# Optimization experiments

Measured on AMD Instinct MI355X. Metric: run time of the kernel, lower is better.

## Reference

```python
import jax, jax.numpy as jnp
import numpy as np
import math

B, S, D, H = 4, 2048, 1024, 16
DK = D // H


def setup_inputs() -> dict:
    key = jax.random.key(0)
    ks = jax.random.split(key, 5)
    stdv_in = math.sqrt(3.0 / (2 * D))
    stdv_out = math.sqrt(1.0 / D)
    return {
        "query": jax.random.normal(ks[0], (B, S, D), dtype=jnp.float32),
        "key": jax.random.normal(ks[1], (B, S, D), dtype=jnp.float32),
        "value": jax.random.normal(ks[2], (B, S, D), dtype=jnp.float32),
        "input_weight": jax.random.uniform(ks[3], (3, D, D), dtype=jnp.float32, minval=-stdv_in, maxval=stdv_in),
        "output_weight": jax.random.uniform(ks[4], (D, D), dtype=jnp.float32, minval=-stdv_out, maxval=stdv_out),
    }


def reference(query, key, value, input_weight, output_weight):
    # x @ W.T, split into heads: (B,S,D) -> (B,H,S,dk)
    def proj(x, w):
        return (x @ w.T).reshape(B, S, H, DK).transpose(0, 2, 1, 3)

    q = proj(query, input_weight[0])
    k = proj(key, input_weight[1])
    v = proj(value, input_weight[2])

    scores = jnp.einsum("bhqd,bhkd->bhqk", q, k) / math.sqrt(DK)  # (B,H,S,S)
    similarity = jax.nn.softmax(scores, axis=-1)
    attn = jnp.einsum("bhqk,bhkd->bhqd", similarity, v)  # (B,H,S,dk)
    attn = attn.transpose(0, 2, 1, 3).reshape(B, S, D)
    attn = attn @ output_weight.T
    # mean_simi_across_heads=True default
    sim_mean = jnp.mean(similarity, axis=1)  # (B,S,S)
    return attn, sim_mean
```

## Files before the change

kernel.cpp:

```cpp
#include <hip/hip_runtime.h>

typedef _Float16 f16x8 __attribute__((ext_vector_type(8)));
typedef _Float16 f16x4 __attribute__((ext_vector_type(4)));
typedef _Float16 f16x2 __attribute__((ext_vector_type(2)));
typedef __fp16 h16x2 __attribute__((ext_vector_type(2)));
typedef float f32x4 __attribute__((ext_vector_type(4)));

#define SWB(row, c8) ((((row) << 3) + (((c8) ^ ((row) & 7)))) << 3)

__device__ __forceinline__ float exp2_fast(float x) {
  return __builtin_amdgcn_exp2f(x);
}

__device__ __forceinline__ f16x2 pkrtz(float a, float b) {
  h16x2 r = __builtin_amdgcn_cvt_pkrtz(a, b);
  return *(f16x2*)&r;
}

__device__ __forceinline__ f16x8 pack8(float4 f0, float4 f1) {
  f16x2 p0 = pkrtz(f0.x, f0.y);
  f16x2 p1 = pkrtz(f0.z, f0.w);
  f16x2 p2 = pkrtz(f1.x, f1.y);
  f16x2 p3 = pkrtz(f1.z, f1.w);
  f16x4 a = __builtin_shufflevector(p0, p1, 0, 1, 2, 3);
  f16x4 b = __builtin_shufflevector(p2, p3, 0, 1, 2, 3);
  return __builtin_shufflevector(a, b, 0, 1, 2, 3, 4, 5, 6, 7);
}

#define LOG2E 1.44269504088896340736f

__global__ __launch_bounds__(256) void conv_kernel(
    const float* __restrict__ q, const float* __restrict__ k,
    const float* __restrict__ v, const float* __restrict__ w_in,
    const float* __restrict__ w_out, _Float16* __restrict__ Xc,
    _Float16* __restrict__ W16, float qscale) {
  int t = blockIdx.x * 256 + threadIdx.x;
  if (t < 3145728) {
    int plane = t >> 20, off = t & 1048575;
    const float* src = (plane == 0 ? q : (plane == 1 ? k : v)) + (size_t)off * 8;
    float4 f0 = *(const float4*)src;
    float4 f1 = *(const float4*)(src + 4);
    *(f16x8*)&Xc[(size_t)t * 8] = pack8(f0, f1);
  } else {
    int t2 = t - 3145728;
    int plane = t2 >> 17, off = t2 & 131071;
    const float* src = (plane < 3 ? w_in + (size_t)plane * 1048576 : w_out) + (size_t)off * 8;
    float sc = (plane == 0) ? qscale : 1.0f;
    float4 f0 = *(const float4*)src;
    float4 f1 = *(const float4*)(src + 4);
    f0.x *= sc; f0.y *= sc; f0.z *= sc; f0.w *= sc;
    f1.x *= sc; f1.y *= sc; f1.z *= sc; f1.w *= sc;
    *(f16x8*)&W16[(size_t)t2 * 8] = pack8(f0, f1);
  }
}

template <int EPI>
__global__ __launch_bounds__(256) void gemm_kernel(const _Float16* __restrict__ A0,
                                                   const _Float16* __restrict__ W16,
                                                   void* Oq, void* Ok, void* Ov) {
  __shared__ _Float16 As[128 * 64];
  __shared__ _Float16 Bs[128 * 64];
  const int tid = threadIdx.x;
  const int w = tid >> 6, lane = tid & 63, quad = lane >> 4, l16 = lane & 15;
  const int m0 = blockIdx.y * 128, n0 = blockIdx.x * 128;
  const int z = blockIdx.z;
  const int wm = (w & 1) * 64, wn = (w >> 1) * 64;
  const int srow = tid >> 3, c8 = tid & 7;

  const _Float16* A = (EPI == 0) ? A0 + (size_t)z * 8388608 : A0;
  const _Float16* W = (EPI == 0) ? W16 + (size_t)z * 1048576 : W16 + (size_t)3 * 1048576;

  f32x4 acc[4][4];
#pragma unroll
  for (int i = 0; i < 4; i++)
#pragma unroll
    for (int j = 0; j < 4; j++) acc[i][j] = (f32x4){0.f, 0.f, 0.f, 0.f};

  f16x8 pa[4], pb[4];
#pragma unroll
  for (int u = 0; u < 4; u++) {
    pa[u] = *(const f16x8*)&A[(size_t)(m0 + srow + 32 * u) * 1024 + c8 * 8];
    pb[u] = *(const f16x8*)&W[(size_t)(n0 + srow + 32 * u) * 1024 + c8 * 8];
  }
#pragma unroll
  for (int u = 0; u < 4; u++) {
    *(f16x8*)&As[SWB(srow + 32 * u, c8)] = pa[u];
    *(f16x8*)&Bs[SWB(srow + 32 * u, c8)] = pb[u];
  }

  for (int k0 = 0; k0 < 1024; k0 += 64) {
    __syncthreads();
    if (k0 < 960) {
      int kn = k0 + 64;
#pragma unroll
      for (int u = 0; u < 4; u++) {
        pa[u] = *(const f16x8*)&A[(size_t)(m0 + srow + 32 * u) * 1024 + kn + c8 * 8];
        pb[u] = *(const f16x8*)&W[(size_t)(n0 + srow + 32 * u) * 1024 + kn + c8 * 8];
      }
    }
    f16x8 af[2][4], bf[2][4];
#pragma unroll
    for (int kf = 0; kf < 2; kf++)
#pragma unroll
      for (int i = 0; i < 4; i++) {
        af[kf][i] = *(f16x8*)&As[SWB(wm + i * 16 + l16, kf * 4 + quad)];
        bf[kf][i] = *(f16x8*)&Bs[SWB(wn + i * 16 + l16, kf * 4 + quad)];
      }
#pragma unroll
    for (int kf = 0; kf < 2; kf++)
#pragma unroll
      for (int i = 0; i < 4; i++)
#pragma unroll
        for (int j = 0; j < 4; j++)
          acc[i][j] = __builtin_amdgcn_mfma_f32_16x16x32_f16(af[kf][i], bf[kf][j], acc[i][j], 0, 0, 0);
    __syncthreads();
    if (k0 < 960) {
#pragma unroll
      for (int u = 0; u < 4; u++) {
        *(f16x8*)&As[SWB(srow + 32 * u, c8)] = pa[u];
        *(f16x8*)&Bs[SWB(srow + 32 * u, c8)] = pb[u];
      }
    }
  }

  if (EPI == 1) {
    float* o = (float*)Oq;
#pragma unroll
    for (int i = 0; i < 4; i++)
#pragma unroll
      for (int j = 0; j < 4; j++)
#pragma unroll
        for (int r = 0; r < 4; r++) {
          int mg = m0 + wm + i * 16 + quad * 4 + r;
          int ng = n0 + wn + j * 16 + l16;
          o[(size_t)mg * 1024 + ng] = acc[i][j][r];
        }
  } else {
    _Float16* o = (_Float16*)(z == 0 ? Oq : (z == 1 ? Ok : Ov));
#pragma unroll
    for (int i = 0; i < 4; i++)
#pragma unroll
      for (int j = 0; j < 4; j++) {
        if (z < 2) {
#pragma unroll
          for (int r = 0; r < 4; r++) {
            int mg = m0 + wm + i * 16 + quad * 4 + r;
            int ng = n0 + wn + j * 16 + l16;
            int bb = mg >> 11, ss = mg & 2047, hh = ng >> 6, dd = ng & 63;
            o[((size_t)(bb * 16 + hh) << 17) + ss * 64 + dd] = (_Float16)acc[i][j][r];
          }
        } else {
          int mg0 = m0 + wm + i * 16 + quad * 4;
          int ng = n0 + wn + j * 16 + l16;
          int bb = mg0 >> 11, ss0 = mg0 & 2047, hh = ng >> 6, dd = ng & 63;
          f16x4 pk;
#pragma unroll
          for (int r = 0; r < 4; r++) pk[r] = (_Float16)acc[i][j][r];
          *(f16x4*)&o[((size_t)(bb * 16 + hh) << 17) + (size_t)dd * 2048 + ss0] = pk;
        }
      }
  }
}

__global__ __launch_bounds__(256) void attn_kernel(const _Float16* __restrict__ Q,
                                                   const _Float16* __restrict__ K,
                                                   const _Float16* __restrict__ Vt,
                                                   _Float16* __restrict__ O,
                                                   float* __restrict__ rl) {
  __shared__ _Float16 Kt[64 * 64];
  __shared__ _Float16 Vtt[64 * 64];
  const int tid = threadIdx.x;
  const int w = tid >> 6, lane = tid & 63, quad = lane >> 4, l16 = lane & 15;
  const int h = blockIdx.y, b = blockIdx.z;
  const size_t base = (size_t)(b * 16 + h) << 17;
  const _Float16* Qh = Q + base;
  const _Float16* Kh = K + base;
  const _Float16* Vth = Vt + base;
  const int q0 = blockIdx.x * 128;
  const int wq = q0 + w * 32;
  const int c0 = tid, c1 = tid + 256;
  const int r0 = c0 >> 3, c80 = c0 & 7, r1 = c1 >> 3, c81 = c1 & 7;
  const int vA0 = (c80 >> 2) * 4 + (c80 & 1) * 2, vh0 = ((c80 >> 1) & 1) * 4;
  const int vA1 = (c81 >> 2) * 4 + (c81 & 1) * 2, vh1 = ((c81 >> 1) & 1) * 4;

  f16x8 aq[2][2];
#pragma unroll
  for (int i = 0; i < 2; i++)
#pragma unroll
    for (int kf = 0; kf < 2; kf++)
      aq[i][kf] = *(const f16x8*)&Qh[(size_t)(wq + i * 16 + l16) * 64 + kf * 32 + quad * 8];

  f32x4 accO[2][4];
  float lsum[2];
#pragma unroll
  for (int i = 0; i < 2; i++) {
    lsum[i] = 0.f;
#pragma unroll
    for (int j = 0; j < 4; j++) accO[i][j] = (f32x4){0.f, 0.f, 0.f, 0.f};
  }
  const f32x4 zero4 = (f32x4){0.f, 0.f, 0.f, 0.f};

  f16x8 kreg[2], vreg[2];
  kreg[0] = *(const f16x8*)&Kh[(size_t)r0 * 64 + c80 * 8];
  kreg[1] = *(const f16x8*)&Kh[(size_t)r1 * 64 + c81 * 8];
  vreg[0] = *(const f16x8*)&Vth[(size_t)r0 * 2048 + c80 * 8];
  vreg[1] = *(const f16x8*)&Vth[(size_t)r1 * 2048 + c81 * 8];
  *(f16x8*)&Kt[SWB(r0, c80)] = kreg[0];
  *(f16x8*)&Kt[SWB(r1, c81)] = kreg[1];
  {
    f16x4 lo0 = __builtin_shufflevector(vreg[0], vreg[0], 0, 1, 2, 3);
    f16x4 hi0 = __builtin_shufflevector(vreg[0], vreg[0], 4, 5, 6, 7);
    *(f16x4*)&Vtt[SWB(r0, vA0) + vh0] = lo0;
    *(f16x4*)&Vtt[SWB(r0, vA0 + 1) + vh0] = hi0;
    f16x4 lo1 = __builtin_shufflevector(vreg[1], vreg[1], 0, 1, 2, 3);
    f16x4 hi1 = __builtin_shufflevector(vreg[1], vreg[1], 4, 5, 6, 7);
    *(f16x4*)&Vtt[SWB(r1, vA1) + vh1] = lo1;
    *(f16x4*)&Vtt[SWB(r1, vA1 + 1) + vh1] = hi1;
  }

  for (int it = 0; it < 32; it++) {
    __syncthreads();
    if (it < 31) {
      int n0 = (it + 1) * 64;
      kreg[0] = *(const f16x8*)&Kh[(size_t)(n0 + r0) * 64 + c80 * 8];
      kreg[1] = *(const f16x8*)&Kh[(size_t)(n0 + r1) * 64 + c81 * 8];
      vreg[0] = *(const f16x8*)&Vth[(size_t)r0 * 2048 + n0 + c80 * 8];
      vreg[1] = *(const f16x8*)&Vth[(size_t)r1 * 2048 + n0 + c81 * 8];
    }
    f16x8 bk[4][2];
#pragma unroll
    for (int jj = 0; jj < 4; jj++)
#pragma unroll
      for (int kf = 0; kf < 2; kf++)
        bk[jj][kf] = *(f16x8*)&Kt[SWB(jj * 16 + l16, kf * 4 + quad)];
    f32x4 sv[2][4];
#pragma unroll
    for (int i = 0; i < 2; i++)
#pragma unroll
      for (int jj = 0; jj < 4; jj++) {
        f32x4 t = __builtin_amdgcn_mfma_f32_16x16x32_f16(bk[jj][0], aq[i][0], zero4, 0, 0, 0);
        sv[i][jj] = __builtin_amdgcn_mfma_f32_16x16x32_f16(bk[jj][1], aq[i][1], t, 0, 0, 0);
      }
    f16x8 ap[2][2];
#pragma unroll
    for (int i = 0; i < 2; i++)
#pragma unroll
      for (int kf = 0; kf < 2; kf++)
#pragma unroll
        for (int hi = 0; hi < 2; hi++)
#pragma unroll
          for (int r = 0; r < 4; r++) {
            float p = exp2_fast(sv[i][2 * kf + hi][r]);
            lsum[i] += p;
            ap[i][kf][hi * 4 + r] = (_Float16)p;
          }
    f16x8 bv[4][2];
#pragma unroll
    for (int jd = 0; jd < 4; jd++)
#pragma unroll
      for (int kf = 0; kf < 2; kf++)
        bv[jd][kf] = *(f16x8*)&Vtt[SWB(jd * 16 + l16, kf * 4 + quad)];
#pragma unroll
    for (int i = 0; i < 2; i++)
#pragma unroll
      for (int jd = 0; jd < 4; jd++) {
        accO[i][jd] = __builtin_amdgcn_mfma_f32_16x16x32_f16(ap[i][0], bv[jd][0], accO[i][jd], 0, 0, 0);
        accO[i][jd] = __builtin_amdgcn_mfma_f32_16x16x32_f16(ap[i][1], bv[jd][1], accO[i][jd], 0, 0, 0);
      }
    __syncthreads();
    if (it < 31) {
      *(f16x8*)&Kt[SWB(r0, c80)] = kreg[0];
      *(f16x8*)&Kt[SWB(r1, c81)] = kreg[1];
      f16x4 lo0 = __builtin_shufflevector(vreg[0], vreg[0], 0, 1, 2, 3);
      f16x4 hi0 = __builtin_shufflevector(vreg[0], vreg[0], 4, 5, 6, 7);
      *(f16x4*)&Vtt[SWB(r0, vA0) + vh0] = lo0;
      *(f16x4*)&Vtt[SWB(r0, vA0 + 1) + vh0] = hi0;
      f16x4 lo1 = __builtin_shufflevector(vreg[1], vreg[1], 0, 1, 2, 3);
      f16x4 hi1 = __builtin_shufflevector(vreg[1], vreg[1], 4, 5, 6, 7);
      *(f16x4*)&Vtt[SWB(r1, vA1) + vh1] = lo1;
      *(f16x4*)&Vtt[SWB(r1, vA1 + 1) + vh1] = hi1;
    }
  }

  float rinv[2];
#pragma unroll
  for (int i = 0; i < 2; i++) {
    float v = lsum[i];
    v += __shfl_xor(v, 16);
    v += __shfl_xor(v, 32);
    rinv[i] = 1.0f / v;
  }
  if (lane < 16) {
#pragma unroll
    for (int i = 0; i < 2; i++)
      rl[(b * 16 + h) * 2048 + wq + i * 16 + lane] = rinv[i];
  }
  float rO[2][4];
#pragma unroll
  for (int i = 0; i < 2; i++)
#pragma unroll
    for (int r = 0; r < 4; r++)
      rO[i][r] = __shfl(rinv[i], quad * 4 + r);

#pragma unroll
  for (int i = 0; i < 2; i++)
#pragma unroll
    for (int jd = 0; jd < 4; jd++)
#pragma unroll
      for (int r = 0; r < 4; r++) {
        int rowq = wq + i * 16 + quad * 4 + r;
        O[(size_t)(b * 2048 + rowq) * 1024 + h * 64 + jd * 16 + l16] =
            (_Float16)(accO[i][jd][r] * rO[i][r]);
      }
}

__global__ __launch_bounds__(512) void sim_kernel(const _Float16* __restrict__ Q,
                                                  const _Float16* __restrict__ K,
                                                  const float* __restrict__ rl,
                                                  float* __restrict__ out) {
  __shared__ _Float16 Ks[128 * 64];
  const int tid = threadIdx.x;
  const int w = tid >> 6, lane = tid & 63, quad = lane >> 4, l16 = lane & 15;
  const int n0 = blockIdx.x * 128, q0 = blockIdx.y * 128, b = blockIdx.z;
  const f32x4 zero4 = (f32x4){0.f, 0.f, 0.f, 0.f};
  const int c0 = tid, c1 = tid + 512;
  const int r0 = c0 >> 3, c80 = c0 & 7, r1 = c1 >> 3, c81 = c1 & 7;

  f32x4 acc[8];
#pragma unroll
  for (int jj = 0; jj < 8; jj++) acc[jj] = (f32x4){0.f, 0.f, 0.f, 0.f};

  f16x8 kreg[2];
  kreg[0] = *(const f16x8*)&K[((size_t)(b * 16) << 17) + (size_t)(n0 + r0) * 64 + c80 * 8];
  kreg[1] = *(const f16x8*)&K[((size_t)(b * 16) << 17) + (size_t)(n0 + r1) * 64 + c81 * 8];
  *(f16x8*)&Ks[SWB(r0, c80)] = kreg[0];
  *(f16x8*)&Ks[SWB(r1, c81)] = kreg[1];

  for (int h = 0; h < 16; h++) {
    __syncthreads();
    if (h < 15) {
      const size_t kb = (size_t)(b * 16 + h + 1) << 17;
      kreg[0] = *(const f16x8*)&K[kb + (size_t)(n0 + r0) * 64 + c80 * 8];
      kreg[1] = *(const f16x8*)&K[kb + (size_t)(n0 + r1) * 64 + c81 * 8];
    }
    const size_t qb = ((size_t)(b * 16 + h) << 17) + (size_t)(q0 + w * 16 + l16) * 64;
    f16x8 aq0 = *(const f16x8*)&Q[qb + quad * 8];
    f16x8 aq1 = *(const f16x8*)&Q[qb + 32 + quad * 8];
    float rv[4];
#pragma unroll
    for (int r = 0; r < 4; r++)
      rv[r] = rl[(b * 16 + h) * 2048 + q0 + w * 16 + quad * 4 + r];
#pragma unroll
    for (int jj = 0; jj < 8; jj++) {
      f16x8 b0 = *(f16x8*)&Ks[SWB(jj * 16 + l16, quad)];
      f16x8 b1 = *(f16x8*)&Ks[SWB(jj * 16 + l16, 4 + quad)];
      f32x4 sv = __builtin_amdgcn_mfma_f32_16x16x32_f16(aq0, b0, zero4, 0, 0, 0);
      sv = __builtin_amdgcn_mfma_f32_16x16x32_f16(aq1, b1, sv, 0, 0, 0);
#pragma unroll
      for (int r = 0; r < 4; r++) acc[jj][r] += exp2_fast(sv[r]) * rv[r];
    }
    __syncthreads();
    if (h < 15) {
      *(f16x8*)&Ks[SWB(r0, c80)] = kreg[0];
      *(f16x8*)&Ks[SWB(r1, c81)] = kreg[1];
    }
  }
#pragma unroll
  for (int jj = 0; jj < 8; jj++)
#pragma unroll
    for (int r = 0; r < 4; r++) {
      int rowq = q0 + w * 16 + quad * 4 + r;
      out[(size_t)(b * 2048 + rowq) * 2048 + n0 + jj * 16 + l16] = acc[jj][r] * 0.0625f;
    }
}

extern "C" void kernel_launch(void* const* d_in, const int* in_sizes, int n_in,
                              void* d_out, int out_size, void* d_ws, size_t ws_size,
                              hipStream_t stream) {
  const float* q = (const float*)d_in[0];
  const float* k = (const float*)d_in[1];
  const float* v = (const float*)d_in[2];
  const float* w_in = (const float*)d_in[3];
  const float* w_out = (const float*)d_in[4];

  _Float16* Qw = (_Float16*)d_ws;
  _Float16* Kw = Qw + 8388608;
  _Float16* Vt = Kw + 8388608;
  _Float16* Ow = Vt + 8388608;
  float* rlw = (float*)(Ow + 8388608);

  float* out_attn = (float*)d_out;
  float* out_sim = out_attn + 8388608;
  _Float16* Xc = (_Float16*)out_sim;
  _Float16* W16 = Xc + 3 * 8388608;

  conv_kernel<<<14336, 256, 0, stream>>>(q, k, v, w_in, w_out, Xc, W16,
                                         0.125f * LOG2E);
  gemm_kernel<0><<<dim3(8, 64, 3), 256, 0, stream>>>(Xc, W16, Qw, Kw, Vt);
  attn_kernel<<<dim3(16, 16, 4), 256, 0, stream>>>(Qw, Kw, Vt, Ow, rlw);
  gemm_kernel<1><<<dim3(8, 64, 1), 256, 0, stream>>>(Ow, W16, out_attn, nullptr, nullptr);
  sim_kernel<<<dim3(16, 16, 4), 512, 0, stream>>>(Qw, Kw, rlw, out_sim);
}
```

Before: 468.3 us.

## Double-buffer K/V shared tiles and compute softmax row sums via MFMA

Both the attention and similarity kernels switch to double-buffered shared memory, so the next tile is staged into one buffer while compute reads the other, with global loads prefetched further ahead. The attention kernel also computes the softmax denominator by multiplying the packed f16 probabilities against a ones vector with MFMA, replacing per-element VALU adds and the cross-lane shuffles for normalization. The cost is doubled LDS use, which may reduce occupancy, and the sums now use f16-rounded probabilities.

```diff
diff --git a/kernel.cpp b/kernel.cpp
--- a/kernel.cpp
+++ b/kernel.cpp
@@ -167,8 +167,8 @@
                                                    const _Float16* __restrict__ Vt,
                                                    _Float16* __restrict__ O,
                                                    float* __restrict__ rl) {
-  __shared__ _Float16 Kt[64 * 64];
-  __shared__ _Float16 Vtt[64 * 64];
+  __shared__ _Float16 KtS[2 * 64 * 64];
+  __shared__ _Float16 VtS[2 * 64 * 64];
   const int tid = threadIdx.x;
   const int w = tid >> 6, lane = tid & 63, quad = lane >> 4, l16 = lane & 15;
   const int h = blockIdx.y, b = blockIdx.z;
@@ -191,48 +191,44 @@
       aq[i][kf] = *(const f16x8*)&Qh[(size_t)(wq + i * 16 + l16) * 64 + kf * 32 + quad * 8];
 
   f32x4 accO[2][4];
-  float lsum[2];
+  f32x4 accL[2];
 #pragma unroll
   for (int i = 0; i < 2; i++) {
-    lsum[i] = 0.f;
+    accL[i] = (f32x4){0.f, 0.f, 0.f, 0.f};
 #pragma unroll
     for (int j = 0; j < 4; j++) accO[i][j] = (f32x4){0.f, 0.f, 0.f, 0.f};
   }
   const f32x4 zero4 = (f32x4){0.f, 0.f, 0.f, 0.f};
+  const f16x8 ones8 = (f16x8){(_Float16)1.f, (_Float16)1.f, (_Float16)1.f, (_Float16)1.f,
+                              (_Float16)1.f, (_Float16)1.f, (_Float16)1.f, (_Float16)1.f};
 
   f16x8 kreg[2], vreg[2];
-  kreg[0] = *(const f16x8*)&Kh[(size_t)r0 * 64 + c80 * 8];
-  kreg[1] = *(const f16x8*)&Kh[(size_t)r1 * 64 + c81 * 8];
-  vreg[0] = *(const f16x8*)&Vth[(size_t)r0 * 2048 + c80 * 8];
-  vreg[1] = *(const f16x8*)&Vth[(size_t)r1 * 2048 + c81 * 8];
-  *(f16x8*)&Kt[SWB(r0, c80)] = kreg[0];
-  *(f16x8*)&Kt[SWB(r1, c81)] = kreg[1];
-  {
+  auto loadkv = [&](int t) {
+    int n0 = t * 64;
+    kreg[0] = *(const f16x8*)&Kh[(size_t)(n0 + r0) * 64 + c80 * 8];
+    kreg[1] = *(const f16x8*)&Kh[(size_t)(n0 + r1) * 64 + c81 * 8];
+    vreg[0] = *(const f16x8*)&Vth[(size_t)r0 * 2048 + n0 + c80 * 8];
+    vreg[1] = *(const f16x8*)&Vth[(size_t)r1 * 2048 + n0 + c81 * 8];
+  };
+  auto stage = [&](_Float16* Kb, _Float16* Vb) {
+    *(f16x8*)&Kb[SWB(r0, c80)] = kreg[0];
+    *(f16x8*)&Kb[SWB(r1, c81)] = kreg[1];
     f16x4 lo0 = __builtin_shufflevector(vreg[0], vreg[0], 0, 1, 2, 3);
     f16x4 hi0 = __builtin_shufflevector(vreg[0], vreg[0], 4, 5, 6, 7);
-    *(f16x4*)&Vtt[SWB(r0, vA0) + vh0] = lo0;
-    *(f16x4*)&Vtt[SWB(r0, vA0 + 1) + vh0] = hi0;
+    *(f16x4*)&Vb[SWB(r0, vA0) + vh0] = lo0;
+    *(f16x4*)&Vb[SWB(r0, vA0 + 1) + vh0] = hi0;
     f16x4 lo1 = __builtin_shufflevector(vreg[1], vreg[1], 0, 1, 2, 3);
     f16x4 hi1 = __builtin_shufflevector(vreg[1], vreg[1], 4, 5, 6, 7);
-    *(f16x4*)&Vtt[SWB(r1, vA1) + vh1] = lo1;
-    *(f16x4*)&Vtt[SWB(r1, vA1 + 1) + vh1] = hi1;
-  }
-
-  for (int it = 0; it < 32; it++) {
-    __syncthreads();
-    if (it < 31) {
-      int n0 = (it + 1) * 64;
-      kreg[0] = *(const f16x8*)&Kh[(size_t)(n0 + r0) * 64 + c80 * 8];
-      kreg[1] = *(const f16x8*)&Kh[(size_t)(n0 + r1) * 64 + c81 * 8];
-      vreg[0] = *(const f16x8*)&Vth[(size_t)r0 * 2048 + n0 + c80 * 8];
-      vreg[1] = *(const f16x8*)&Vth[(size_t)r1 * 2048 + n0 + c81 * 8];
-    }
+    *(f16x4*)&Vb[SWB(r1, vA1) + vh1] = lo1;
+    *(f16x4*)&Vb[SWB(r1, vA1 + 1) + vh1] = hi1;
+  };
+  auto compute = [&](const _Float16* Kb, const _Float16* Vb) {
     f16x8 bk[4][2];
 #pragma unroll
     for (int jj = 0; jj < 4; jj++)
 #pragma unroll
       for (int kf = 0; kf < 2; kf++)
-        bk[jj][kf] = *(f16x8*)&Kt[SWB(jj * 16 + l16, kf * 4 + quad)];
+        bk[jj][kf] = *(const f16x8*)&Kb[SWB(jj * 16 + l16, kf * 4 + quad)];
     f32x4 sv[2][4];
 #pragma unroll
     for (int i = 0; i < 2; i++)
@@ -243,23 +239,29 @@
       }
     f16x8 ap[2][2];
 #pragma unroll
-    for (int i = 0; i < 2; i++)
+    for (int i = 0; i < 2; i++) {
+#pragma unroll
+      for (int kf = 0; kf < 2; kf++) {
+        float4 e0, e1;
+        e0.x = exp2_fast(sv[i][2 * kf][0]);
+        e0.y = exp2_fast(sv[i][2 * kf][1]);
+        e0.z = exp2_fast(sv[i][2 * kf][2]);
+        e0.w = exp2_fast(sv[i][2 * kf][3]);
+        e1.x = exp2_fast(sv[i][2 * kf + 1][0]);
+        e1.y = exp2_fast(sv[i][2 * kf + 1][1]);
+        e1.z = exp2_fast(sv[i][2 * kf + 1][2]);
+        e1.w = exp2_fast(sv[i][2 * kf + 1][3]);
+        ap[i][kf] = pack8(e0, e1);
+      }
+      accL[i] = __builtin_amdgcn_mfma_f32_16x16x32_f16(ap[i][0], ones8, accL[i], 0, 0, 0);
+      accL[i] = __builtin_amdgcn_mfma_f32_16x16x32_f16(ap[i][1], ones8, accL[i], 0, 0, 0);
+    }
+    f16x8 bv[4][2];
+#pragma unroll
+    for (int jd = 0; jd < 4; jd++)
 #pragma unroll
       for (int kf = 0; kf < 2; kf++)
-#pragma unroll
-        for (int hi = 0; hi < 2; hi++)
-#pragma unroll
-          for (int r = 0; r < 4; r++) {
-            float p = exp2_fast(sv[i][2 * kf + hi][r]);
-            lsum[i] += p;
-            ap[i][kf][hi * 4 + r] = (_Float16)p;
-          }
-    f16x8 bv[4][2];
-#pragma unroll
-    for (int jd = 0; jd < 4; jd++)
-#pragma unroll
-      for (int kf = 0; kf < 2; kf++)
-        bv[jd][kf] = *(f16x8*)&Vtt[SWB(jd * 16 + l16, kf * 4 + quad)];
+        bv[jd][kf] = *(const f16x8*)&Vb[SWB(jd * 16 + l16, kf * 4 + quad)];
 #pragma unroll
     for (int i = 0; i < 2; i++)
 #pragma unroll
@@ -267,41 +269,36 @@
         accO[i][jd] = __builtin_amdgcn_mfma_f32_16x16x32_f16(ap[i][0], bv[jd][0], accO[i][jd], 0, 0, 0);
         accO[i][jd] = __builtin_amdgcn_mfma_f32_16x16x32_f16(ap[i][1], bv[jd][1], accO[i][jd], 0, 0, 0);
       }
-    __syncthreads();
-    if (it < 31) {
-      *(f16x8*)&Kt[SWB(r0, c80)] = kreg[0];
-      *(f16x8*)&Kt[SWB(r1, c81)] = kreg[1];
-      f16x4 lo0 = __builtin_shufflevector(vreg[0], vreg[0], 0, 1, 2, 3);
-      f16x4 hi0 = __builtin_shufflevector(vreg[0], vreg[0], 4, 5, 6, 7);
-      *(f16x4*)&Vtt[SWB(r0, vA0) + vh0] = lo0;
-      *(f16x4*)&Vtt[SWB(r0, vA0 + 1) + vh0] = hi0;
-      f16x4 lo1 = __builtin_shufflevector(vreg[1], vreg[1], 0, 1, 2, 3);
-      f16x4 hi1 = __builtin_shufflevector(vreg[1], vreg[1], 4, 5, 6, 7);
-      *(f16x4*)&Vtt[SWB(r1, vA1) + vh1] = lo1;
-      *(f16x4*)&Vtt[SWB(r1, vA1 + 1) + vh1] = hi1;
-    }
-  }
-
-  float rinv[2];
-#pragma unroll
-  for (int i = 0; i < 2; i++) {
-    float v = lsum[i];
-    v += __shfl_xor(v, 16);
-    v += __shfl_xor(v, 32);
-    rinv[i] = 1.0f / v;
-  }
-  if (lane < 16) {
+  };
+
+  loadkv(0);
+  stage(&KtS[0], &VtS[0]);
+  loadkv(1);
+  for (int it2 = 0; it2 < 16; ++it2) {
+    __syncthreads();
+    stage(&KtS[4096], &VtS[4096]);
+    if (it2 < 15) loadkv(2 * it2 + 2);
+    compute(&KtS[0], &VtS[0]);
+    __syncthreads();
+    if (it2 < 15) {
+      stage(&KtS[0], &VtS[0]);
+      loadkv(2 * it2 + 3);
+    }
+    compute(&KtS[4096], &VtS[4096]);
+  }
+
+  float rinv[2][4];
+#pragma unroll
+  for (int i = 0; i < 2; i++)
+#pragma unroll
+    for (int r = 0; r < 4; r++) rinv[i][r] = 1.0f / accL[i][r];
+  if (l16 == 0) {
 #pragma unroll
     for (int i = 0; i < 2; i++)
-      rl[(b * 16 + h) * 2048 + wq + i * 16 + lane] = rinv[i];
-  }
-  float rO[2][4];
-#pragma unroll
-  for (int i = 0; i < 2; i++)
-#pragma unroll
-    for (int r = 0; r < 4; r++)
-      rO[i][r] = __shfl(rinv[i], quad * 4 + r);
-
+#pragma unroll
+      for (int r = 0; r < 4; r++)
+        rl[(b * 16 + h) * 2048 + wq + i * 16 + quad * 4 + r] = rinv[i][r];
+  }
 #pragma unroll
   for (int i = 0; i < 2; i++)
 #pragma unroll
@@ -310,7 +307,7 @@
       for (int r = 0; r < 4; r++) {
         int rowq = wq + i * 16 + quad * 4 + r;
         O[(size_t)(b * 2048 + rowq) * 1024 + h * 64 + jd * 16 + l16] =
-            (_Float16)(accO[i][jd][r] * rO[i][r]);
+            (_Float16)(accO[i][jd][r] * rinv[i][r]);
       }
 }
 
@@ -318,7 +315,7 @@
                                                   const _Float16* __restrict__ K,
                                                   const float* __restrict__ rl,
                                                   float* __restrict__ out) {
-  __shared__ _Float16 Ks[128 * 64];
+  __shared__ _Float16 Ks[2 * 128 * 64];
   const int tid = threadIdx.x;
   const int w = tid >> 6, lane = tid & 63, quad = lane >> 4, l16 = lane & 15;
   const int n0 = blockIdx.x * 128, q0 = blockIdx.y * 128, b = blockIdx.z;
@@ -331,39 +328,48 @@
   for (int jj = 0; jj < 8; jj++) acc[jj] = (f32x4){0.f, 0.f, 0.f, 0.f};
 
   f16x8 kreg[2];
-  kreg[0] = *(const f16x8*)&K[((size_t)(b * 16) << 17) + (size_t)(n0 + r0) * 64 + c80 * 8];
-  kreg[1] = *(const f16x8*)&K[((size_t)(b * 16) << 17) + (size_t)(n0 + r1) * 64 + c81 * 8];
-  *(f16x8*)&Ks[SWB(r0, c80)] = kreg[0];
-  *(f16x8*)&Ks[SWB(r1, c81)] = kreg[1];
-
-  for (int h = 0; h < 16; h++) {
-    __syncthreads();
-    if (h < 15) {
-      const size_t kb = (size_t)(b * 16 + h + 1) << 17;
-      kreg[0] = *(const f16x8*)&K[kb + (size_t)(n0 + r0) * 64 + c80 * 8];
-      kreg[1] = *(const f16x8*)&K[kb + (size_t)(n0 + r1) * 64 + c81 * 8];
-    }
-    const size_t qb = ((size_t)(b * 16 + h) << 17) + (size_t)(q0 + w * 16 + l16) * 64;
+  auto loadK = [&](int hh) {
+    const size_t kb = (size_t)(b * 16 + hh) << 17;
+    kreg[0] = *(const f16x8*)&K[kb + (size_t)(n0 + r0) * 64 + c80 * 8];
+    kreg[1] = *(const f16x8*)&K[kb + (size_t)(n0 + r1) * 64 + c81 * 8];
+  };
+  auto stageK = [&](_Float16* Kb) {
+    *(f16x8*)&Kb[SWB(r0, c80)] = kreg[0];
+    *(f16x8*)&Kb[SWB(r1, c81)] = kreg[1];
+  };
+  auto computeS = [&](int hh, const _Float16* Kb) {
+    const size_t qb = ((size_t)(b * 16 + hh) << 17) + (size_t)(q0 + w * 16 + l16) * 64;
     f16x8 aq0 = *(const f16x8*)&Q[qb + quad * 8];
     f16x8 aq1 = *(const f16x8*)&Q[qb + 32 + quad * 8];
     float rv[4];
 #pragma unroll
     for (int r = 0; r < 4; r++)
-      rv[r] = rl[(b * 16 + h) * 2048 + q0 + w * 16 + quad * 4 + r];
+      rv[r] = rl[(b * 16 + hh) * 2048 + q0 + w * 16 + quad * 4 + r];
 #pragma unroll
     for (int jj = 0; jj < 8; jj++) {
-      f16x8 b0 = *(f16x8*)&Ks[SWB(jj * 16 + l16, quad)];
-      f16x8 b1 = *(f16x8*)&Ks[SWB(jj * 16 + l16, 4 + quad)];
+      f16x8 b0 = *(const f16x8*)&Kb[SWB(jj * 16 + l16, quad)];
+      f16x8 b1 = *(const f16x8*)&Kb[SWB(jj * 16 + l16, 4 + quad)];
       f32x4 sv = __builtin_amdgcn_mfma_f32_16x16x32_f16(aq0, b0, zero4, 0, 0, 0);
       sv = __builtin_amdgcn_mfma_f32_16x16x32_f16(aq1, b1, sv, 0, 0, 0);
 #pragma unroll
       for (int r = 0; r < 4; r++) acc[jj][r] += exp2_fast(sv[r]) * rv[r];
     }
-    __syncthreads();
-    if (h < 15) {
-      *(f16x8*)&Ks[SWB(r0, c80)] = kreg[0];
-      *(f16x8*)&Ks[SWB(r1, c81)] = kreg[1];
-    }
+  };
+
+  loadK(0);
+  stageK(&Ks[0]);
+  loadK(1);
+  for (int h2 = 0; h2 < 8; ++h2) {
+    __syncthreads();
+    stageK(&Ks[8192]);
+    if (h2 < 7) loadK(2 * h2 + 2);
+    computeS(2 * h2, &Ks[0]);
+    __syncthreads();
+    if (h2 < 7) {
+      stageK(&Ks[0]);
+      loadK(2 * h2 + 3);
+    }
+    computeS(2 * h2 + 1, &Ks[8192]);
   }
 #pragma unroll
   for (int jj = 0; jj < 8; jj++)
```

Result: faster. 435.2 us (-7.1%).
